# Optimization experiments

Hardware: AMD Instinct MI355X
Metric: run time of the kernel (lower is better)

## Reference

```python
import jax, jax.numpy as jnp
import numpy as np

# NOTE: the repo's helpers quantum_attention_weights / von_neumann_entropy are not in the
# snippet; they are reconstructed from the standard decoherence model used by this repo:
#   rho = p |psi><psi| + (1-p) I/d  (Born rule attention weight = <m|rho|m> = p|<m|psi>|^2 + (1-p)/d)
# Metrics (entropies, detached attn) are no-grad diagnostics and omitted; reference returns `out`.

B, N, D, H, HD, S = 8, 2048, 1024, 8, 128, 64  # HD = hilbert_dim


def setup_inputs() -> dict:
    key = jax.random.key(0)
    ks = jax.random.split(key, 12)
    f = lambda k, shp: jax.random.normal(k, shp, dtype=jnp.float32)
    return {
        "h": f(ks[0], (B, N, D)),
        "W_real": f(ks[1], (H, D, HD)) * 0.02,
        "W_imag": f(ks[2], (H, D, HD)) * 0.02,
        "p_w1": f(ks[3], (H, D, 16)) * (1.0 / np.sqrt(D)),
        "p_b1": jnp.zeros((H, 16), jnp.float32),
        "p_w2": f(ks[4], (H, 16, 1)) * 0.25,
        "p_b2": jnp.zeros((H, 1), jnp.float32),
        "m_real": f(ks[5], (H, S, HD)) * (1.0 / np.sqrt(HD)),
        "m_imag": f(ks[6], (H, S, HD)) * (1.0 / np.sqrt(HD)),
        "values": f(ks[7], (H, S, D)) * 0.02,
        "gate_w": f(ks[8], (H * D, H)) * (1.0 / np.sqrt(H * D)),
        "gate_b": jnp.zeros((H,), jnp.float32),
        "out_w": f(ks[9], (D, D)) * (1.0 / np.sqrt(D)),
        "out_b": jnp.zeros((D,), jnp.float32),
    }


def reference(h, W_real, W_imag, p_w1, p_b1, p_w2, p_b2,
              m_real, m_imag, values, gate_w, gate_b, out_w, out_b):
    d = W_real.shape[-1]
    # complex per-head projection |psi>: (B,H,N,d), L2-normalized over d
    re = jnp.einsum('bnD,hDe->bhne', h, W_real)
    im = jnp.einsum('bnD,hDe->bhne', h, W_imag)
    psi = (re + 1j * im).astype(jnp.complex64)
    psi = psi / jnp.maximum(jnp.linalg.norm(psi, axis=-1, keepdims=True), 1e-12)
    # per-head purity/decoherence prob p in (0, 0.95): small MLP on h
    hid = jax.nn.silu(jnp.einsum('bnD,hDk->bhnk', h, p_w1) + p_b1[None, :, None, :])
    p = jax.nn.sigmoid(jnp.einsum('bhnk,hko->bhno', hid, p_w2)
                       + p_b2[None, :, None, :])[..., 0] * 0.95  # (B,H,N)
    # normalized complex memory states (H,S,d)
    mem = (m_real + 1j * m_imag).astype(jnp.complex64)
    mem = mem / jnp.maximum(jnp.linalg.norm(mem, axis=-1, keepdims=True), 1e-12)
    # Born-rule overlaps with decohered state: p*|<m|psi>|^2 + (1-p)/d
    ov = jnp.einsum('bhne,hse->bhns', psi, jnp.conj(mem))
    overlap = jnp.real(ov) ** 2 + jnp.imag(ov) ** 2  # (B,H,N,S)
    raw = p[..., None] * overlap + (1.0 - p[..., None]) / d
    attn = raw / (jnp.sum(raw, axis=-1, keepdims=True) + 1e-8)
    # per-head value aggregation -> (B,N,H,D)
    outs = jnp.einsum('bhns,hsD->bnhD', attn, values)
    b, n, nh, dd = outs.shape
    gates = jax.nn.softmax(outs.reshape(b, n, nh * dd) @ gate_w + gate_b, axis=-1)  # (B,N,H)
    combined = jnp.einsum('bnhD,bnh->bnD', outs, gates)
    return combined @ out_w + out_b
```

## Files before the change

### kernel.cpp

```cpp
#include <hip/hip_runtime.h>
#include <hip/hip_bf16.h>
#include <math.h>

#define ROWS 16384

typedef _Float16 f16x8 __attribute__((ext_vector_type(8)));
typedef float f32x4 __attribute__((ext_vector_type(4)));

static const size_t OFF_OVL = 0;
static const size_t OFF_HID = 8388608;
static const size_t OFF_N2  = 10485760;
static const size_t OFF_VG  = 10616832;
static const size_t OFF_MRE = 10620928;
static const size_t OFF_MIM = 10686464;
static const size_t OFF_VWH = 10752000;
static const size_t OFF_VWL = 11014144;
static const size_t OFF_BH  = 11276288;
static const size_t OFF_BL  = 12914688;
static const size_t OFF_AH  = 14553088;
static const size_t OFF_AL  = 22941696;
static const size_t WS_FLOATS = 31330304;

__device__ __forceinline__ void gload_lds16(const void* g, void* l) {
  __builtin_amdgcn_global_load_lds((const __attribute__((address_space(1))) void*)g,
                                   (__attribute__((address_space(3))) void*)l, 16, 0, 0);
}

__device__ __forceinline__ void split16(float v, _Float16& hi, _Float16& lo) {
  _Float16 h = (_Float16)v;
  hi = h;
  lo = (_Float16)(v - (float)h);
}

__global__ __launch_bounds__(256) void k_prep_all(const float* __restrict__ h_,
                                                  const float* __restrict__ Wr,
                                                  const float* __restrict__ Wi,
                                                  const float* __restrict__ pw1,
                                                  const float* __restrict__ mr,
                                                  const float* __restrict__ mi,
                                                  const float* __restrict__ vals,
                                                  const float* __restrict__ gw,
                                                  const float* __restrict__ ow,
                                                  float* __restrict__ VG,
                                                  _Float16* __restrict__ BH,
                                                  _Float16* __restrict__ BL,
                                                  _Float16* __restrict__ VWH,
                                                  _Float16* __restrict__ VWL,
                                                  _Float16* __restrict__ AH,
                                                  _Float16* __restrict__ AL) {
  __shared__ __align__(16) char pbuf[33024];
  const int b = blockIdx.x;
  const int tid = threadIdx.x;

  if (b < 128) {
    int sub = b;
    int col0 = (sub & 15) << 6, row0 = (sub >> 4) << 6;
    float (*As)[64] = (float(*)[64])pbuf;
    float (*Bs)[64] = (float(*)[64])(pbuf + 4096);
    int tm = tid >> 4, tn = tid & 15;
    float acc[4][4];
    #pragma unroll
    for (int i = 0; i < 4; ++i)
      #pragma unroll
      for (int j = 0; j < 4; ++j) acc[i][j] = 0.f;
    int ar = tid >> 2, ak = (tid & 3) << 2;
    int bkr = tid >> 4, bc = (tid & 15) << 2;
    for (int kt = 0; kt < 1024; kt += 16) {
      float4 a0 = *(const float4*)(vals + (size_t)(row0 + ar)*1024 + kt + ak);
      float4 b0 = *(const float4*)(ow + (size_t)(kt + bkr)*1024 + col0 + bc);
      __syncthreads();
      As[ak+0][ar] = a0.x; As[ak+1][ar] = a0.y; As[ak+2][ar] = a0.z; As[ak+3][ar] = a0.w;
      *(float4*)&Bs[bkr][bc] = b0;
      __syncthreads();
      #pragma unroll
      for (int k = 0; k < 16; ++k) {
        float af[4], bf[4];
        *(float4*)&af[0] = *(const float4*)&As[k][tm << 2];
        *(float4*)&bf[0] = *(const float4*)&Bs[k][tn << 2];
        #pragma unroll
        for (int i = 0; i < 4; ++i)
          #pragma unroll
          for (int j = 0; j < 4; ++j) acc[i][j] += af[i] * bf[j];
      }
    }
    #pragma unroll
    for (int i = 0; i < 4; ++i) {
      int row = row0 + (tm << 2) + i;
      int ktl = row >> 5, kg = (row >> 3) & 3, jj = row & 7;
      #pragma unroll
      for (int j = 0; j < 4; ++j) {
        int col = col0 + (tn << 2) + j;
        int nt = col >> 7, c8 = (col >> 4) & 7, c15 = col & 15;
        size_t base = ((size_t)nt*16 + ktl)*4096 + c8*512 + kg*128 + c15*8 + jj;
        _Float16 hi, lo; split16(acc[i][j], hi, lo);
        VWH[base] = hi; VWL[base] = lo;
      }
    }

  } else if (b < 384) {
    int bid = b - 128;
    int h   = bid >> 5;
    int kt64 = (bid >> 1) & 15;
    int sh  = bid & 1;
    float (*sRe)[129] = (float(*)[129])pbuf;
    float (*sIm)[129] = (float(*)[129])(pbuf + 16512);
    int s0 = sh * 32;
    for (int i = tid; i < 32 * 32; i += 256) {
      int s = i >> 5; int e4 = (i & 31) << 2;
      *(float4*)&sRe[s][e4] = *(const float4*)(mr + ((size_t)(h*64 + s0 + s)*128 + e4));
      *(float4*)&sIm[s][e4] = *(const float4*)(mi + ((size_t)(h*64 + s0 + s)*128 + e4));
    }
    __syncthreads();
    {
      int row = tid >> 3, part = tid & 7;
      float ss = 0.f;
      #pragma unroll
      for (int e = 0; e < 16; ++e) {
        float a = sRe[row][part*16 + e], bb = sIm[row][part*16 + e];
        ss += a*a + bb*bb;
      }
      ss += __shfl_xor(ss, 1); ss += __shfl_xor(ss, 2); ss += __shfl_xor(ss, 4);
      float inv = 1.f / fmaxf(sqrtf(ss), 1e-12f);
      #pragma unroll
      for (int e = 0; e < 16; ++e) {
        sRe[row][part*16 + e] *= inv;
        sIm[row][part*16 + e] *= inv;
      }
    }
    __syncthreads();
    int kq = tid >> 5;
    int s  = tid & 31;
    int kbase = kt64*64 + kq*8;
    float aR[8] = {0,0,0,0,0,0,0,0}, aI[8] = {0,0,0,0,0,0,0,0};
    for (int e0 = 0; e0 < 128; e0 += 4) {
      float4 mre = *(float4*)&sRe[s][e0];
      float4 mim = *(float4*)&sIm[s][e0];
      #pragma unroll
      for (int j = 0; j < 8; ++j) {
        const float4 wr = *(const float4*)(Wr + ((size_t)(h*1024 + kbase + j))*128 + e0);
        const float4 wi = *(const float4*)(Wi + ((size_t)(h*1024 + kbase + j))*128 + e0);
        aR[j] += wr.x*mre.x + wr.y*mre.y + wr.z*mre.z + wr.w*mre.w
               + wi.x*mim.x + wi.y*mim.y + wi.z*mim.z + wi.w*mim.w;
        aI[j] += wi.x*mre.x + wi.y*mre.y + wi.z*mre.z + wi.w*mre.w
               - (wr.x*mim.x + wr.y*mim.y + wr.z*mim.z + wr.w*mim.w);
      }
    }
    int kt32 = kbase >> 5;
    int kg   = (kbase >> 3) & 3;
    int coln = s0 + s;
    size_t baseR = ((size_t)(16 + h)*32 + kt32)*4096 + (size_t)(coln >> 4)*512 + kg*128 + (coln & 15)*8;
    size_t baseI = baseR + 4*512;
    f16x8 hR, lR, hI, lI;
    #pragma unroll
    for (int j = 0; j < 8; ++j) {
      _Float16 hi, lo;
      split16(aR[j], hi, lo); hR[j] = hi; lR[j] = lo;
      split16(aI[j], hi, lo); hI[j] = hi; lI[j] = lo;
    }
    *(f16x8*)(BH + baseR) = hR; *(f16x8*)(BL + baseR) = lR;
    *(f16x8*)(BH + baseI) = hI; *(f16x8*)(BL + baseI) = lI;

  } else if (b < 896) {
    int hs = b - 384;
    int h  = hs >> 6;
    float acc[8] = {0,0,0,0,0,0,0,0};
    for (int dd = tid; dd < 1024; dd += 256) {
      float v = vals[(size_t)hs*1024 + dd];
      const float* g = gw + (size_t)(h*1024 + dd)*8;
      #pragma unroll
      for (int q = 0; q < 8; ++q) acc[q] += v * g[q];
    }
    #pragma unroll
    for (int off = 1; off < 64; off <<= 1)
      #pragma unroll
      for (int q = 0; q < 8; ++q) acc[q] += __shfl_xor(acc[q], off);
    float* red = (float*)pbuf;
    if ((tid & 63) == 0) {
      #pragma unroll
      for (int q = 0; q < 8; ++q) red[(tid >> 6)*8 + q] = acc[q];
    }
    __syncthreads();
    if (tid < 8) VG[(size_t)hs*8 + tid] = red[tid] + red[8 + tid] + red[16 + tid] + red[24 + tid];

  } else if (b < 1984) {
    int g = (b - 896) * 256 + tid;
    int c  = g % 2176;
    int k0 = g / 2176;
    float v[8];
    if (c < 1024) {
      int h = c >> 7, e = c & 127;
      const float* p = Wr + ((size_t)(h << 10) + k0*8) * 128 + e;
      #pragma unroll
      for (int j = 0; j < 8; ++j) v[j] = p[(size_t)j*128];
    } else if (c < 2048) {
      int c2 = c - 1024; int h = c2 >> 7, e = c2 & 127;
      const float* p = Wi + ((size_t)(h << 10) + k0*8) * 128 + e;
      #pragma unroll
      for (int j = 0; j < 8; ++j) v[j] = p[(size_t)j*128];
    } else {
      int q = c - 2048; int h = q >> 4, kk = q & 15;
      const float* p = pw1 + ((size_t)(h << 10) + k0*8) * 16 + kk;
      #pragma unroll
      for (int j = 0; j < 8; ++j) v[j] = p[(size_t)j*16];
    }
    int Bcol = (c < 2048) ? c : 3072 + (c - 2048);
    int nt = Bcol >> 7, c8 = (Bcol >> 4) & 7, c15 = Bcol & 15;
    int kt = k0 >> 2, kg = k0 & 3;
    size_t base = ((size_t)nt*32 + kt)*4096 + c8*512 + kg*128 + c15*8;
    f16x8 hv, lv;
    #pragma unroll
    for (int j = 0; j < 8; ++j) { _Float16 hi, lo; split16(v[j], hi, lo); hv[j] = hi; lv[j] = lo; }
    *(f16x8*)(BH + base) = hv;
    *(f16x8*)(BL + base) = lv;

  } else {
    int cb = b - 1984;
    int mt = cb >> 5, kt = cb & 31;
    size_t tbase = (size_t)cb * 4096;
    #pragma unroll
    for (int it = 0; it < 2; ++it) {
      int p = it*256 + tid;
      int r8 = p >> 6, kg = (p >> 4) & 3, r15 = p & 15;
      int row = mt*128 + r8*16 + r15;
      int col = kt*32 + kg*8;
      const float* s = h_ + (size_t)row*1024 + col;
      float4 v0 = *(const float4*)s;
      float4 v1 = *(const float4*)(s + 4);
      float vv[8] = {v0.x, v0.y, v0.z, v0.w, v1.x, v1.y, v1.z, v1.w};
      f16x8 hv, lv;
      #pragma unroll
      for (int j = 0; j < 8; ++j) { _Float16 hi, lo; split16(vv[j], hi, lo); hv[j] = hi; lv[j] = lo; }
      size_t i = tbase + (size_t)r8*512 + kg*128 + r15*8;
      *(f16x8*)(AH + i) = hv;
      *(f16x8*)(AL + i) = lv;
    }
  }
}

__global__ __launch_bounds__(256) void k_qmm(const _Float16* __restrict__ Ah,
                                             const _Float16* __restrict__ Al,
                                             const _Float16* __restrict__ Bh,
                                             const _Float16* __restrict__ Bl,
                                             float* __restrict__ OVL,
                                             float* __restrict__ HID,
                                             float* __restrict__ n2a,
                                             float* __restrict__ n2b) {
  __shared__ __align__(16) char smem[65536];
  const int gid = blockIdx.x;
  const int tid = threadIdx.x;
  const int wid = tid >> 6, lane = tid & 63;
  const int wr = wid >> 1, wc = wid & 1;

  if (gid < 1152) {
    const int id = gid;
    const int rest = id >> 3;
    const int by = (id & 7) * 16 + (rest & 15);
    const int bx = rest >> 4;
    f32x4 acc[4][4];
    #pragma unroll
    for (int i = 0; i < 4; ++i)
      #pragma unroll
      for (int j = 0; j < 4; ++j) acc[i][j] = (f32x4){0.f,0.f,0.f,0.f};

    const char* pAh = (const char*)Ah + (size_t)by*32*8192;
    const char* pAl = (const char*)Al + (size_t)by*32*8192;
    const char* pBh = (const char*)Bh + (size_t)(16 + bx)*32*8192;
    const char* pBl = (const char*)Bl + (size_t)(16 + bx)*32*8192;
    const char* mysrc = (wid == 0) ? pAh : (wid == 1) ? pAl : (wid == 2) ? pBh : pBl;

    auto stage = [&](int b, int kt) {
      const char* s = mysrc + (size_t)kt*8192 + lane*16;
      char* d = smem + b*32768 + wid*8192;
      #pragma unroll
      for (int q = 0; q < 8; ++q)
        gload_lds16(s + q*1024, d + q*1024);
    };

    stage(0, 0);
    asm volatile("s_waitcnt vmcnt(0)" ::: "memory");
    __builtin_amdgcn_s_barrier();
    int cur = 0;
    for (int kt = 0; kt < 32; ++kt) {
      if (kt < 31) stage(cur ^ 1, kt + 1);
      const char* base = smem + cur*32768;
      const char* cAh = base;
      const char* cAl = base + 8192;
      const char* cBh = base + 16384;
      const char* cBl = base + 24576;
      f16x8 a_h[4], a_l[4], b_h[4], b_l[4];
      #pragma unroll
      for (int m = 0; m < 4; ++m) { a_h[m] = *(const f16x8*)(cAh + wr*4096 + m*1024 + lane*16);
                                    a_l[m] = *(const f16x8*)(cAl + wr*4096 + m*1024 + lane*16); }
      #pragma unroll
      for (int n = 0; n < 4; ++n) { b_h[n] = *(const f16x8*)(cBh + wc*4096 + n*1024 + lane*16);
                                    b_l[n] = *(const f16x8*)(cBl + wc*4096 + n*1024 + lane*16); }
      #pragma unroll
      for (int m = 0; m < 4; ++m)
        #pragma unroll
        for (int n = 0; n < 4; ++n) {
          acc[m][n] = __builtin_amdgcn_mfma_f32_16x16x32_f16(a_h[m], b_h[n], acc[m][n], 0, 0, 0);
          acc[m][n] = __builtin_amdgcn_mfma_f32_16x16x32_f16(a_l[m], b_h[n], acc[m][n], 0, 0, 0);
          acc[m][n] = __builtin_amdgcn_mfma_f32_16x16x32_f16(a_h[m], b_l[n], acc[m][n], 0, 0, 0);
        }
      if (kt < 31) {
        asm volatile("s_waitcnt vmcnt(0)" ::: "memory");
        __builtin_amdgcn_s_barrier();
      }
      cur ^= 1;
    }
    __syncthreads();

    if (bx == 8) {
      #pragma unroll
      for (int m = 0; m < 4; ++m)
        #pragma unroll
        for (int n = 0; n < 4; ++n)
          #pragma unroll
          for (int rr = 0; rr < 4; ++rr) {
            int row = by*128 + wr*64 + m*16 + (lane>>4)*4 + rr;
            int col = wc*64 + n*16 + (lane&15);
            HID[(size_t)row*128 + col] = acc[m][n][rr];
          }
    } else {
      float* sOv = (float*)smem;
      if (wc == 0) {
        #pragma unroll
        for (int m = 0; m < 4; ++m)
          #pragma unroll
          for (int n = 0; n < 4; ++n)
            #pragma unroll
            for (int rr = 0; rr < 4; ++rr) {
              int r128 = wr*64 + m*16 + (lane>>4)*4 + rr;
              int s = n*16 + (lane&15);
              sOv[r128*68 + s] = acc[m][n][rr]*acc[m][n][rr];
            }
      }
      __syncthreads();
      if (wc == 1) {
        #pragma unroll
        for (int m = 0; m < 4; ++m)
          #pragma unroll
          for (int n = 0; n < 4; ++n)
            #pragma unroll
            for (int rr = 0; rr < 4; ++rr) {
              int r128 = wr*64 + m*16 + (lane>>4)*4 + rr;
              int s = n*16 + (lane&15);
              float v = sOv[r128*68 + s] + acc[m][n][rr]*acc[m][n][rr];
              int row = by*128 + r128;
              OVL[(size_t)row*512 + bx*64 + s] = v;
            }
      }
    }

  } else {
    const int id = gid - 1152;
    const int by = (id & 7) * 16 + ((id >> 3) & 15);
    const int bx = id >> 7;
    const char* gA  = (const char*)Ah + (size_t)by * 32 * 8192;
    const char* gB0 = (const char*)Bh + (size_t)(2*bx)     * 32 * 8192;
    const char* gB1 = (const char*)Bh + (size_t)(2*bx + 1) * 32 * 8192;

    f32x4 acc[4][8];
    #pragma unroll
    for (int i = 0; i < 4; ++i)
      #pragma unroll
      for (int j = 0; j < 8; ++j) acc[i][j] = (f32x4){0.f,0.f,0.f,0.f};

    auto stage = [&](int b, int kt) {
      char* dbuf = smem + b * 24576;
      #pragma unroll
      for (int q = 0; q < 6; ++q) {
        int c = wid * 6 + q;
        const char* s;
        if (c < 8)       s = gA  + (size_t)kt*8192 + c*1024;
        else if (c < 16) s = gB0 + (size_t)kt*8192 + (c-8)*1024;
        else             s = gB1 + (size_t)kt*8192 + (c-16)*1024;
        gload_lds16(s + lane*16, dbuf + c*1024);
      }
    };

    stage(0, 0);
    stage(1, 1);
    asm volatile("s_waitcnt vmcnt(6)" ::: "memory");
    __builtin_amdgcn_s_barrier();
    for (int kt = 0; kt < 32; ++kt) {
      const char* cb = smem + (kt & 1) * 24576;
      const char* bb = cb + 8192 + wc * 8192;
      f16x8 a[4], b[8];
      #pragma unroll
      for (int m = 0; m < 4; ++m) a[m] = *(const f16x8*)(cb + wr*4096 + m*1024 + lane*16);
      #pragma unroll
      for (int n = 0; n < 8; ++n) b[n] = *(const f16x8*)(bb + n*1024 + lane*16);
      asm volatile("s_waitcnt lgkmcnt(0)" ::: "memory");
      __builtin_amdgcn_s_barrier();
      if (kt < 30) stage(kt & 1, kt + 2);
      #pragma unroll
      for (int m = 0; m < 4; ++m)
        #pragma unroll
        for (int n = 0; n < 8; ++n)
          acc[m][n] = __builtin_amdgcn_mfma_f32_16x16x32_f16(a[m], b[n], acc[m][n], 0, 0, 0);
      if (kt < 31) {
        if (kt < 30) asm volatile("s_waitcnt vmcnt(6)" ::: "memory");
        else         asm volatile("s_waitcnt vmcnt(0)" ::: "memory");
        __builtin_amdgcn_s_barrier();
      }
    }

    const int nt = 2*bx + wc;
    float* dst = (nt < 8) ? n2a : n2b;
    const int head = nt & 7;
    #pragma unroll
    for (int m = 0; m < 4; ++m)
      #pragma unroll
      for (int rr = 0; rr < 4; ++rr) {
        float rs = 0.f;
        #pragma unroll
        for (int n = 0; n < 8; ++n) rs += acc[m][n][rr] * acc[m][n][rr];
        rs += __shfl_xor(rs, 1); rs += __shfl_xor(rs, 2);
        rs += __shfl_xor(rs, 4); rs += __shfl_xor(rs, 8);
        if ((lane & 15) == 0) {
          int row = by*128 + wr*64 + m*16 + (lane >> 4)*4 + rr;
          dst[(size_t)row*8 + head] = rs;
        }
      }
  }
}

__global__ __launch_bounds__(256) void k_fin(const _Float16* __restrict__ Ahh,
                                             const _Float16* __restrict__ Alo,
                                             const _Float16* __restrict__ Bhh,
                                             const _Float16* __restrict__ Blo,
                                             const float* __restrict__ bias,
                                             float* __restrict__ out) {
  __shared__ __align__(16) char smem[65536];
  const int id = blockIdx.x;
  const int by = (id & 7) * 16 + ((id >> 3) & 15);
  const int bx = id >> 7;
  const int tid = threadIdx.x;
  const int wid = tid >> 6, lane = tid & 63;
  const int wr = wid >> 1, wc = wid & 1;
  f32x4 acc[4][4];
  #pragma unroll
  for (int i = 0; i < 4; ++i)
    #pragma unroll
    for (int j = 0; j < 4; ++j) acc[i][j] = (f32x4){0.f,0.f,0.f,0.f};
  const char* pAh = (const char*)Ahh + (size_t)by*16*8192;
  const char* pAl = (const char*)Alo + (size_t)by*16*8192;
  const char* pBh = (const char*)Bhh + (size_t)bx*16*8192;
  const char* pBl = (const char*)Blo + (size_t)bx*16*8192;
  const char* mysrc = (wid == 0) ? pAh : (wid == 1) ? pAl : (wid == 2) ? pBh : pBl;

  auto stage = [&](int b, int kt) {
    const char* s = mysrc + (size_t)kt*8192 + lane*16;
    char* d = smem + b*32768 + wid*8192;
    #pragma unroll
    for (int q = 0; q < 8; ++q)
      gload_lds16(s + q*1024, d + q*1024);
  };

  stage(0, 0);
  stage(1, 1);
  asm volatile("s_waitcnt vmcnt(8)" ::: "memory");
  __builtin_amdgcn_s_barrier();
  for (int kt = 0; kt < 16; ++kt) {
    const char* base = smem + (kt & 1)*32768;
    const char* cAh = base;
    const char* cAl = base + 8192;
    const char* cBh = base + 16384;
    const char* cBl = base + 24576;
    f16x8 a_h[4], a_l[4], b_h[4], b_l[4];
    #pragma unroll
    for (int m = 0; m < 4; ++m) { a_h[m] = *(const f16x8*)(cAh + wr*4096 + m*1024 + lane*16);
                                  a_l[m] = *(const f16x8*)(cAl + wr*4096 + m*1024 + lane*16); }
    #pragma unroll
    for (int n = 0; n < 4; ++n) { b_h[n] = *(const f16x8*)(cBh + wc*4096 + n*1024 + lane*16);
                                  b_l[n] = *(const f16x8*)(cBl + wc*4096 + n*1024 + lane*16); }
    asm volatile("s_waitcnt lgkmcnt(0)" ::: "memory");
    __builtin_amdgcn_s_barrier();
    if (kt < 14) stage(kt & 1, kt + 2);
    #pragma unroll
    for (int m = 0; m < 4; ++m)
      #pragma unroll
      for (int n = 0; n < 4; ++n) {
        acc[m][n] = __builtin_amdgcn_mfma_f32_16x16x32_f16(a_h[m], b_h[n], acc[m][n], 0, 0, 0);
        acc[m][n] = __builtin_amdgcn_mfma_f32_16x16x32_f16(a_l[m], b_h[n], acc[m][n], 0, 0, 0);
        acc[m][n] = __builtin_amdgcn_mfma_f32_16x16x32_f16(a_h[m], b_l[n], acc[m][n], 0, 0, 0);
      }
    if (kt < 15) {
      if (kt < 14) asm volatile("s_waitcnt vmcnt(8)" ::: "memory");
      else         asm volatile("s_waitcnt vmcnt(0)" ::: "memory");
      __builtin_amdgcn_s_barrier();
    }
  }
  #pragma unroll
  for (int m = 0; m < 4; ++m)
    #pragma unroll
    for (int n = 0; n < 4; ++n) {
      int col = bx*128 + wc*64 + n*16 + (lane&15);
      float bv = bias[col];
      #pragma unroll
      for (int rr = 0; rr < 4; ++rr) {
        int row = by*128 + wr*64 + m*16 + (lane>>4)*4 + rr;
        out[(size_t)row*1024 + col] = acc[m][n][rr] + bv;
      }
    }
}

__global__ __launch_bounds__(256) void k_attn(const float* __restrict__ OVL,
                                              const float* __restrict__ HID,
                                              const float* __restrict__ n2a,
                                              const float* __restrict__ n2b,
                                              const float* __restrict__ VG,
                                              const float* __restrict__ pb1,
                                              const float* __restrict__ pw2,
                                              const float* __restrict__ pb2,
                                              const float* __restrict__ gb,
                                              _Float16* __restrict__ WH,
                                              _Float16* __restrict__ WL) {
  const int wid = threadIdx.x >> 6;
  const int lane = threadIdx.x & 63;
  const int r = blockIdx.x * 4 + wid;
  const int h = lane >> 3;
  const int sub = lane & 7;
  const float* ovp = OVL + (size_t)r*512 + h*64 + sub*8;
  float4 o0 = *(const float4*)ovp;
  float4 o1 = *(const float4*)(ovp + 4);
  float ov[8] = {o0.x, o0.y, o0.z, o0.w, o1.x, o1.y, o1.z, o1.w};
  float z = 0.f;
  #pragma unroll
  for (int t = 0; t < 2; ++t) {
    int kk = sub*2 + t;
    float x = HID[(size_t)r*128 + h*16 + kk] + pb1[h*16 + kk];
    float sg = 1.f / (1.f + expf(-x));
    z += x * sg * pw2[h*16 + kk];
  }
  z += __shfl_xor(z, 1); z += __shfl_xor(z, 2); z += __shfl_xor(z, 4);
  z += pb2[h];
  float p = 0.95f / (1.f + expf(-z));
  float nn = n2a[(size_t)r*8 + h] + n2b[(size_t)r*8 + h];
  float inv_n2 = 1.f / fmaxf(nn, 1e-24f);
  float base = (1.f - p) * 0.0078125f;
  float rw[8];
  float rsum = 0.f;
  #pragma unroll
  for (int q = 0; q < 8; ++q) { rw[q] = p * (ov[q] * inv_n2) + base; rsum += rw[q]; }
  rsum += __shfl_xor(rsum, 1); rsum += __shfl_xor(rsum, 2); rsum += __shfl_xor(rsum, 4);
  float inv_den = 1.f / (rsum + 1e-8f);
  float a[8];
  #pragma unroll
  for (int q = 0; q < 8; ++q) a[q] = rw[q] * inv_den;
  float lg[8] = {0,0,0,0,0,0,0,0};
  const float* vgp = VG + (size_t)(h*64 + sub*8) * 8;
  #pragma unroll
  for (int q = 0; q < 8; ++q)
    #pragma unroll
    for (int g = 0; g < 8; ++g) lg[g] += a[q] * vgp[q*8 + g];
  #pragma unroll
  for (int off = 1; off < 64; off <<= 1)
    #pragma unroll
    for (int g = 0; g < 8; ++g) lg[g] += __shfl_xor(lg[g], off);
  float lt[8];
  #pragma unroll
  for (int g = 0; g < 8; ++g) lt[g] = lg[g] + gb[g];
  float mx = lt[0];
  #pragma unroll
  for (int g = 1; g < 8; ++g) mx = fmaxf(mx, lt[g]);
  float den = 0.f;
  #pragma unroll
  for (int g = 0; g < 8; ++g) den += expf(lt[g] - mx);
  float gate = expf(lt[h] - mx) / den;
  int mt = r >> 7, r8 = (r >> 4) & 7, r15 = r & 15;
  size_t basek = ((size_t)mt*16 + h*2 + (sub >> 2)) * 4096
               + (size_t)r8*512 + (size_t)(sub & 3)*128 + (size_t)r15*8;
  f16x8 hv, lv;
  #pragma unroll
  for (int q = 0; q < 8; ++q) {
    _Float16 hi, lo;
    split16(a[q] * gate, hi, lo);
    hv[q] = hi; lv[q] = lo;
  }
  *(f16x8*)(WH + basek) = hv;
  *(f16x8*)(WL + basek) = lv;
}

extern "C" void kernel_launch(void* const* d_in, const int* in_sizes, int n_in,
                              void* d_out, int out_size, void* d_ws, size_t ws_size,
                              hipStream_t stream) {
  const float* h_   = (const float*)d_in[0];
  const float* Wr   = (const float*)d_in[1];
  const float* Wi   = (const float*)d_in[2];
  const float* pw1  = (const float*)d_in[3];
  const float* pb1  = (const float*)d_in[4];
  const float* pw2  = (const float*)d_in[5];
  const float* pb2  = (const float*)d_in[6];
  const float* mr   = (const float*)d_in[7];
  const float* mi   = (const float*)d_in[8];
  const float* vals = (const float*)d_in[9];
  const float* gw   = (const float*)d_in[10];
  const float* gb   = (const float*)d_in[11];
  const float* ow   = (const float*)d_in[12];
  const float* ob   = (const float*)d_in[13];

  if (ws_size < WS_FLOATS * sizeof(float)) return;

  float* ws   = (float*)d_ws;
  float* OVL  = ws + OFF_OVL;
  float* HID  = ws + OFF_HID;
  float* n2a  = ws + OFF_N2;
  float* n2b  = ws + OFF_MRE;
  float* VG   = ws + OFF_VG;
  _Float16* VWH = (_Float16*)(ws + OFF_VWH);
  _Float16* VWL = (_Float16*)(ws + OFF_VWL);
  _Float16* BH  = (_Float16*)(ws + OFF_BH);
  _Float16* BL  = (_Float16*)(ws + OFF_BL);
  _Float16* AH  = (_Float16*)(ws + OFF_AH);
  _Float16* AL  = (_Float16*)(ws + OFF_AL);
  _Float16* WH  = (_Float16*)(ws + OFF_AH);
  _Float16* WL  = (_Float16*)(ws + OFF_AL);

  k_prep_all<<<6080, 256, 0, stream>>>(h_, Wr, Wi, pw1, mr, mi, vals, gw, ow,
                                       VG, BH, BL, VWH, VWL, AH, AL);
  k_qmm<<<2176, 256, 0, stream>>>(AH, AL, BH, BL, OVL, HID, n2a, n2b);
  k_attn<<<4096, 256, 0, stream>>>(OVL, HID, n2a, n2b, VG, pb1, pw2, pb2, gb, WH, WL);
  k_fin<<<1024, 256, 0, stream>>>(WH, WL, VWH, VWL, ob, (float*)d_out);
}
```

Measured before the change: 357.7 us.

## Split hidden-layer GEMM into single-pass fp16 blocks and deepen prep K-tile

```diff
diff --git a/kernel.cpp b/kernel.cpp
--- a/kernel.cpp
+++ b/kernel.cpp
@@ -56,24 +56,28 @@
     int sub = b;
     int col0 = (sub & 15) << 6, row0 = (sub >> 4) << 6;
     float (*As)[64] = (float(*)[64])pbuf;
-    float (*Bs)[64] = (float(*)[64])(pbuf + 4096);
+    float (*Bs)[64] = (float(*)[64])(pbuf + 8192);
     int tm = tid >> 4, tn = tid & 15;
     float acc[4][4];
     #pragma unroll
     for (int i = 0; i < 4; ++i)
       #pragma unroll
       for (int j = 0; j < 4; ++j) acc[i][j] = 0.f;
-    int ar = tid >> 2, ak = (tid & 3) << 2;
+    int ar = tid >> 2, ak = (tid & 3) << 3;
     int bkr = tid >> 4, bc = (tid & 15) << 2;
-    for (int kt = 0; kt < 1024; kt += 16) {
+    for (int kt = 0; kt < 1024; kt += 32) {
       float4 a0 = *(const float4*)(vals + (size_t)(row0 + ar)*1024 + kt + ak);
+      float4 a1 = *(const float4*)(vals + (size_t)(row0 + ar)*1024 + kt + ak + 4);
       float4 b0 = *(const float4*)(ow + (size_t)(kt + bkr)*1024 + col0 + bc);
+      float4 b1 = *(const float4*)(ow + (size_t)(kt + 16 + bkr)*1024 + col0 + bc);
       __syncthreads();
       As[ak+0][ar] = a0.x; As[ak+1][ar] = a0.y; As[ak+2][ar] = a0.z; As[ak+3][ar] = a0.w;
-      *(float4*)&Bs[bkr][bc] = b0;
+      As[ak+4][ar] = a1.x; As[ak+5][ar] = a1.y; As[ak+6][ar] = a1.z; As[ak+7][ar] = a1.w;
+      *(float4*)&Bs[bkr][bc]      = b0;
+      *(float4*)&Bs[bkr + 16][bc] = b1;
       __syncthreads();
       #pragma unroll
-      for (int k = 0; k < 16; ++k) {
+      for (int k = 0; k < 32; ++k) {
         float af[4], bf[4];
         *(float4*)&af[0] = *(const float4*)&As[k][tm << 2];
         *(float4*)&bf[0] = *(const float4*)&Bs[k][tn << 2];
@@ -251,11 +255,10 @@
   const int wid = tid >> 6, lane = tid & 63;
   const int wr = wid >> 1, wc = wid & 1;
 
-  if (gid < 1152) {
+  if (gid < 1024) {
     const int id = gid;
-    const int rest = id >> 3;
-    const int by = (id & 7) * 16 + (rest & 15);
-    const int bx = rest >> 4;
+    const int by = (id & 7) * 16 + ((id >> 3) & 15);
+    const int bx = id >> 7;
     f32x4 acc[4][4];
     #pragma unroll
     for (int i = 0; i < 4; ++i)
@@ -310,50 +313,37 @@
     }
     __syncthreads();
 
-    if (bx == 8) {
+    float* sOv = (float*)smem;
+    if (wc == 0) {
       #pragma unroll
       for (int m = 0; m < 4; ++m)
         #pragma unroll
         for (int n = 0; n < 4; ++n)
           #pragma unroll
           for (int rr = 0; rr < 4; ++rr) {
-            int row = by*128 + wr*64 + m*16 + (lane>>4)*4 + rr;
-            int col = wc*64 + n*16 + (lane&15);
-            HID[(size_t)row*128 + col] = acc[m][n][rr];
+            int r128 = wr*64 + m*16 + (lane>>4)*4 + rr;
+            int s = n*16 + (lane&15);
+            sOv[r128*68 + s] = acc[m][n][rr]*acc[m][n][rr];
           }
-    } else {
-      float* sOv = (float*)smem;
-      if (wc == 0) {
-        #pragma unroll
-        for (int m = 0; m < 4; ++m)
+    }
+    __syncthreads();
+    if (wc == 1) {
+      #pragma unroll
+      for (int m = 0; m < 4; ++m)
+        #pragma unroll
+        for (int n = 0; n < 4; ++n)
           #pragma unroll
-          for (int n = 0; n < 4; ++n)
-            #pragma unroll
-            for (int rr = 0; rr < 4; ++rr) {
-              int r128 = wr*64 + m*16 + (lane>>4)*4 + rr;
-              int s = n*16 + (lane&15);
-              sOv[r128*68 + s] = acc[m][n][rr]*acc[m][n][rr];
-            }
-      }
-      __syncthreads();
-      if (wc == 1) {
-        #pragma unroll
-        for (int m = 0; m < 4; ++m)
-          #pragma unroll
-          for (int n = 0; n < 4; ++n)
-            #pragma unroll
-            for (int rr = 0; rr < 4; ++rr) {
-              int r128 = wr*64 + m*16 + (lane>>4)*4 + rr;
-              int s = n*16 + (lane&15);
-              float v = sOv[r128*68 + s] + acc[m][n][rr]*acc[m][n][rr];
-              int row = by*128 + r128;
-              OVL[(size_t)row*512 + bx*64 + s] = v;
-            }
-      }
-    }
-
-  } else {
-    const int id = gid - 1152;
+          for (int rr = 0; rr < 4; ++rr) {
+            int r128 = wr*64 + m*16 + (lane>>4)*4 + rr;
+            int s = n*16 + (lane&15);
+            float v = sOv[r128*68 + s] + acc[m][n][rr]*acc[m][n][rr];
+            int row = by*128 + r128;
+            OVL[(size_t)row*512 + bx*64 + s] = v;
+          }
+    }
+
+  } else if (gid < 2048) {
+    const int id = gid - 1024;
     const int by = (id & 7) * 16 + ((id >> 3) & 15);
     const int bx = id >> 7;
     const char* gA  = (const char*)Ah + (size_t)by * 32 * 8192;
@@ -423,6 +413,63 @@
           dst[(size_t)row*8 + head] = rs;
         }
       }
+
+  } else {
+    const int id = gid - 2048;
+    const int by = (id & 7) * 16 + ((id >> 3) & 15);
+    const char* pAh = (const char*)Ah + (size_t)by*32*8192;
+    const char* pBh = (const char*)Bh + (size_t)24*32*8192;
+    f32x4 acc[4][4];
+    #pragma unroll
+    for (int i = 0; i < 4; ++i)
+      #pragma unroll
+      for (int j = 0; j < 4; ++j) acc[i][j] = (f32x4){0.f,0.f,0.f,0.f};
+
+    auto stage = [&](int b, int kt) {
+      char* dbuf = smem + b*16384;
+      #pragma unroll
+      for (int q = 0; q < 4; ++q) {
+        int c = wid*4 + q;
+        const char* s = (c < 8) ? pAh + (size_t)kt*8192 + c*1024
+                                : pBh + (size_t)kt*8192 + (c-8)*1024;
+        gload_lds16(s + lane*16, dbuf + c*1024);
+      }
+    };
+
+    stage(0, 0);
+    asm volatile("s_waitcnt vmcnt(0)" ::: "memory");
+    __builtin_amdgcn_s_barrier();
+    int cur = 0;
+    for (int kt = 0; kt < 32; ++kt) {
+      if (kt < 31) stage(cur ^ 1, kt + 1);
+      const char* cAh = smem + cur*16384;
+      const char* cBh = cAh + 8192;
+      f16x8 a_h[4], b_h[4];
+      #pragma unroll
+      for (int m = 0; m < 4; ++m) a_h[m] = *(const f16x8*)(cAh + wr*4096 + m*1024 + lane*16);
+      #pragma unroll
+      for (int n = 0; n < 4; ++n) b_h[n] = *(const f16x8*)(cBh + wc*4096 + n*1024 + lane*16);
+      #pragma unroll
+      for (int m = 0; m < 4; ++m)
+        #pragma unroll
+        for (int n = 0; n < 4; ++n)
+          acc[m][n] = __builtin_amdgcn_mfma_f32_16x16x32_f16(a_h[m], b_h[n], acc[m][n], 0, 0, 0);
+      if (kt < 31) {
+        asm volatile("s_waitcnt vmcnt(0)" ::: "memory");
+        __builtin_amdgcn_s_barrier();
+      }
+      cur ^= 1;
+    }
+    #pragma unroll
+    for (int m = 0; m < 4; ++m)
+      #pragma unroll
+      for (int n = 0; n < 4; ++n)
+        #pragma unroll
+        for (int rr = 0; rr < 4; ++rr) {
+          int row = by*128 + wr*64 + m*16 + (lane>>4)*4 + rr;
+          int col = wc*64 + n*16 + (lane&15);
+          HID[(size_t)row*128 + col] = acc[m][n][rr];
+        }
   }
 }
 
```

Result: faster. 329.4 us, median of 2 (-7.9%).
